# Kernel optimization log

Measured on AMD Instinct MI355X. Metric: run time of the kernel, lower is better.

The kernel has to match this reference:

```python
import jax, jax.numpy as jnp
import numpy as np

B, S, D = 2, 2048, 1024
H, HD = 16, 64  # num_heads, head_dim; H*HD == D


def setup_inputs() -> dict:
    key = jax.random.key(0)
    ks = jax.random.split(key, 10)
    scale = 1.0 / np.sqrt(D)
    inputs_q = jax.random.normal(ks[0], (B, S, D), dtype=jnp.float32)
    inputs_kv = inputs_q  # self-attention
    Wq = jax.random.normal(ks[1], (D, H, HD), dtype=jnp.float32) * scale
    Wk = jax.random.normal(ks[2], (D, H, HD), dtype=jnp.float32) * scale
    Wv = jax.random.normal(ks[3], (D, H, HD), dtype=jnp.float32) * scale
    Wo = jax.random.normal(ks[4], (H, HD, D), dtype=jnp.float32) * scale
    bq = jnp.zeros((H, HD), dtype=jnp.float32)
    bk = jnp.zeros((H, HD), dtype=jnp.float32)
    bv = jnp.zeros((H, HD), dtype=jnp.float32)
    bo = jnp.zeros((D,), dtype=jnp.float32)
    return {"inputs_q": inputs_q, "inputs_kv": inputs_kv,
            "Wq": Wq, "bq": bq, "Wk": Wk, "bk": bk,
            "Wv": Wv, "bv": bv, "Wo": Wo, "bo": bo}


def reference(inputs_q, inputs_kv, Wq, bq, Wk, bk, Wv, bv, Wo, bo):
    # QKV projections: [B,S,D] x [D,H,HD] -> [B,S,H,HD]
    q = jnp.einsum('bsd,dhe->bshe', inputs_q, Wq) + bq
    k = jnp.einsum('bsd,dhe->bshe', inputs_kv, Wk) + bk
    v = jnp.einsum('bsd,dhe->bshe', inputs_kv, Wv) + bv
    # scale query by sqrt(depth) as in dot_product_attention
    q = q / jnp.sqrt(jnp.asarray(HD, dtype=q.dtype))
    # attention scores: [B,H,Sq,Sk]
    scores = jnp.einsum('bqhd,bkhd->bhqk', q, k)
    weights = jax.nn.softmax(scores, axis=-1)
    # weighted values: [B,Sq,H,HD]
    ctx = jnp.einsum('bhqk,bkhd->bqhd', weights, v)
    # output projection over (head, head_dim) axes
    out = jnp.einsum('bqhd,hde->bqe', ctx, Wo) + bo
    return out
```

## Files before the change

kernel.cpp:

```cpp
#include <hip/hip_runtime.h>
#include <hip/hip_bf16.h>

typedef __bf16 bf16x8 __attribute__((ext_vector_type(8)));
typedef __bf16 bf16x4 __attribute__((ext_vector_type(4)));
typedef float f32x4 __attribute__((ext_vector_type(4)));

#define MFMA(a,b,c) __builtin_amdgcn_mfma_f32_16x16x32_bf16(a,b,c,0,0,0)

__device__ __forceinline__ unsigned short f2bf(float f) {
    union { float f; unsigned u; } x; x.f = f;
    unsigned r = x.u + 0x7fffu + ((x.u >> 16) & 1u);
    return (unsigned short)(r >> 16);
}

__device__ __forceinline__ bf16x8 ld8(const unsigned short* p) {
    return *reinterpret_cast<const bf16x8*>(p);
}

__device__ __forceinline__ float exp2_fast(float x) {
    float r; asm("v_exp_f32 %0, %1" : "=v"(r) : "v"(x)); return r;
}

__device__ __forceinline__ void stage16(const unsigned short* g, unsigned short* l) {
    __builtin_amdgcn_global_load_lds(
        (const __attribute__((address_space(1))) unsigned int*)(const void*)(g),
        (__attribute__((address_space(3))) unsigned int*)(void*)(l),
        16, 0, 0);
}

__global__ void k_cvt(const float* __restrict__ in, unsigned short* __restrict__ out, int n4) {
    int i = blockIdx.x * blockDim.x + threadIdx.x;
    int stride = gridDim.x * blockDim.x;
    for (; i < n4; i += stride) {
        float4 v = reinterpret_cast<const float4*>(in)[i];
        ushort4 o;
        o.x = f2bf(v.x); o.y = f2bf(v.y); o.z = f2bf(v.z); o.w = f2bf(v.w);
        reinterpret_cast<ushort4*>(out)[i] = o;
    }
}

__global__ void k_cvt_t(const float* __restrict__ in, unsigned short* __restrict__ out) {
    __shared__ unsigned short tile[64][66];
    int t = threadIdx.x;
    int bk = (blockIdx.x & 15) * 64, bn = (blockIdx.x >> 4) * 64;
    #pragma unroll
    for (int r = 0; r < 16; ++r) {
        int k = (t >> 6) * 16 + r;
        int n = t & 63;
        tile[n][k] = f2bf(in[(bk + k) * 1024 + bn + n]);
    }
    __syncthreads();
    #pragma unroll
    for (int r = 0; r < 16; ++r) {
        int n = (t >> 6) * 16 + r;
        int k = t & 63;
        out[(bn + n) * 1024 + bk + k] = tile[n][k];
    }
}

template<int EPI>
__global__ __launch_bounds__(256) void k_gemm_s(
    const unsigned short* __restrict__ A,
    const unsigned short* __restrict__ Bt,
    const float* __restrict__ b0, const float* __restrict__ b1,
    const float* __restrict__ b2,
    unsigned short* __restrict__ q_out, unsigned short* __restrict__ k_out,
    unsigned short* __restrict__ v_out, float* __restrict__ f_out,
    int M, int N, int K)
{
    __shared__ __align__(16) unsigned short A_lds[2][128][32];
    __shared__ __align__(16) unsigned short B_lds[2][128][32];

    const int lane = threadIdx.x & 63;
    const int wave = threadIdx.x >> 6;
    const int wr = wave >> 1, wc = wave & 1;
    const int nbm = M >> 7;
    const int nwg = nbm * (N >> 7);
    int blk = blockIdx.x;
    blk = (blk & 7) * (nwg >> 3) + (blk >> 3);
    const int bm = (blk % nbm) << 7;
    const int bn = (blk / nbm) << 7;
    const int g = lane >> 4, r16 = lane & 15;

    const int srow = lane >> 2;
    const int schunk = lane & 3;
    const unsigned short* Asrc = A  + (size_t)(bm + wave * 32 + srow) * K + schunk * 8;
    const unsigned short* Bsrc = Bt + (size_t)(bn + wave * 32 + srow) * K + schunk * 8;

    auto stage = [&](int buf, int k0) {
        #pragma unroll
        for (int j = 0; j < 2; ++j) {
            stage16(Asrc + (size_t)(j * 16) * K + k0, &A_lds[buf][wave * 32 + j * 16][0]);
            stage16(Bsrc + (size_t)(j * 16) * K + k0, &B_lds[buf][wave * 32 + j * 16][0]);
        }
    };

    f32x4 acc[4][4] = {};

    stage(0, 0);
    __syncthreads();

    const int nsteps = K >> 5;
    for (int t = 0; t < nsteps; ++t) {
        const int cur = t & 1;
        if (t + 1 < nsteps) stage(cur ^ 1, (t + 1) * 32);

        bf16x8 a[4], b[4];
        #pragma unroll
        for (int i = 0; i < 4; ++i)
            a[i] = ld8(&A_lds[cur][wr * 64 + i * 16 + r16][g * 8]);
        #pragma unroll
        for (int j = 0; j < 4; ++j)
            b[j] = ld8(&B_lds[cur][wc * 64 + j * 16 + r16][g * 8]);
        #pragma unroll
        for (int i = 0; i < 4; ++i)
            #pragma unroll
            for (int j = 0; j < 4; ++j)
                acc[i][j] = MFMA(a[i], b[j], acc[i][j]);
        __syncthreads();
    }

    const int seg = bn >> 10;
    const float* bias = (EPI == 1) ? b0 : (seg == 0 ? b0 : (seg == 1 ? b1 : b2));
    const float scale = (EPI == 0 && seg == 0) ? 0.18033688011112042f : 1.0f;

    #pragma unroll
    for (int i = 0; i < 4; ++i)
        #pragma unroll
        for (int j = 0; j < 4; ++j) {
            const int mbase = bm + wr * 64 + i * 16 + g * 4;
            const int n = bn + wc * 64 + j * 16 + r16;
            if constexpr (EPI == 1) {
                #pragma unroll
                for (int r = 0; r < 4; ++r)
                    f_out[(size_t)(mbase + r) * N + n] = acc[i][j][r] + b0[n];
            } else {
                const int nl = n & 1023;
                const int h = nl >> 6, e = nl & 63;
                const int b_ = mbase >> 11, s0 = mbase & 2047;
                float vv[4];
                #pragma unroll
                for (int r = 0; r < 4; ++r)
                    vv[r] = (acc[i][j][r] + bias[nl]) * scale;
                if (seg == 2) {
                    bf16x4 pk = { (__bf16)vv[0], (__bf16)vv[1], (__bf16)vv[2], (__bf16)vv[3] };
                    *reinterpret_cast<bf16x4*>(
                        &v_out[(((size_t)(b_ * 16 + h) * 64 + e) * 2048) + s0]) = pk;
                } else {
                    unsigned short* o = (seg == 0) ? q_out : k_out;
                    #pragma unroll
                    for (int r = 0; r < 4; ++r)
                        o[(((size_t)(b_ * 16 + h) * 2048 + (s0 + r)) * 64) + e] = f2bf(vv[r]);
                }
            }
        }
}

__global__ __launch_bounds__(256) void k_attn(
    const unsigned short* __restrict__ Q,
    const unsigned short* __restrict__ Kb,
    const unsigned short* __restrict__ Vt,
    unsigned short* __restrict__ ctx)
{
    __shared__ __align__(16) unsigned short K_lds[2][64][64];
    __shared__ __align__(16) unsigned short V_lds[2][64][64];
    __shared__ __align__(16) unsigned short P_lds[4][32][72];

    const int lane = threadIdx.x & 63;
    const int wave = threadIdx.x >> 6;
    const int g = lane >> 4, r16 = lane & 15;

    const int blk = blockIdx.x;
    const int x = blk & 7, i = blk >> 3;
    const int bh = x * 4 + (i & 3);
    const int qb = i >> 2;
    const int b = bh >> 4, h = bh & 15;
    const int q0 = qb * 128 + wave * 32;

    const unsigned short* Qp    = Q  + ((size_t)bh * 2048 + q0) * 64;
    const unsigned short* Khead = Kb + (size_t)bh * 2048 * 64;
    const unsigned short* Vhead = Vt + (size_t)bh * 64 * 2048;

    bf16x8 aq[2][2];
    #pragma unroll
    for (int m = 0; m < 2; ++m)
        #pragma unroll
        for (int h2 = 0; h2 < 2; ++h2)
            aq[m][h2] = ld8(Qp + (size_t)(m * 16 + r16) * 64 + h2 * 32 + g * 8);

    bf16x8 ones;
    #pragma unroll
    for (int j = 0; j < 8; ++j) ones[j] = (__bf16)1.0f;

    const int srow = lane >> 3;
    const int schunk = (lane & 7) ^ srow;

    auto stage = [&](int buf, int kt) {
        #pragma unroll
        for (int j = 0; j < 2; ++j) {
            const int r0 = wave * 16 + j * 8;
            stage16(Khead + (size_t)(kt + r0 + srow) * 64 + schunk * 8,
                    &K_lds[buf][r0][0]);
            stage16(Vhead + (size_t)(r0 + srow) * 2048 + kt + schunk * 8,
                    &V_lds[buf][r0][0]);
        }
    };

    f32x4 o[2][4] = {};
    f32x4 sum_acc[2] = {};
    const int sw = r16 & 7;

    stage(0, 0);
    __syncthreads();

    for (int it = 0; it < 32; ++it) {
        const int cur = it & 1;
        if (it + 1 < 32) stage(cur ^ 1, (it + 1) * 64);

        f32x4 s[2][4] = {};
        #pragma unroll
        for (int c = 0; c < 4; ++c) {
            bf16x8 bk0 = ld8(&K_lds[cur][c * 16 + r16][((g)     ^ sw) * 8]);
            bf16x8 bk1 = ld8(&K_lds[cur][c * 16 + r16][((4 + g) ^ sw) * 8]);
            #pragma unroll
            for (int m = 0; m < 2; ++m) {
                s[m][c] = MFMA(bk0, aq[m][0], s[m][c]);
                s[m][c] = MFMA(bk1, aq[m][1], s[m][c]);
            }
        }
        bf16x8 bv[4][2];
        #pragma unroll
        for (int n = 0; n < 4; ++n)
            #pragma unroll
            for (int ks = 0; ks < 2; ++ks)
                bv[n][ks] = ld8(&V_lds[cur][n * 16 + r16][((ks * 4 + g) ^ sw) * 8]);

        #pragma unroll
        for (int m = 0; m < 2; ++m) {
            #pragma unroll
            for (int c = 0; c < 4; ++c) {
                float p0 = exp2_fast(s[m][c][0]);
                float p1 = exp2_fast(s[m][c][1]);
                float p2 = exp2_fast(s[m][c][2]);
                float p3 = exp2_fast(s[m][c][3]);
                bf16x4 pk = { (__bf16)p0, (__bf16)p1, (__bf16)p2, (__bf16)p3 };
                *reinterpret_cast<bf16x4*>(&P_lds[wave][m * 16 + r16][c * 16 + g * 4]) = pk;
            }
        }
        #pragma unroll
        for (int m = 0; m < 2; ++m) {
            bf16x8 ap0 = ld8(&P_lds[wave][m * 16 + r16][g * 8]);
            bf16x8 ap1 = ld8(&P_lds[wave][m * 16 + r16][32 + g * 8]);
            #pragma unroll
            for (int n = 0; n < 4; ++n) {
                o[m][n] = MFMA(ap0, bv[n][0], o[m][n]);
                o[m][n] = MFMA(ap1, bv[n][1], o[m][n]);
            }
            sum_acc[m] = MFMA(ap0, ones, sum_acc[m]);
            sum_acc[m] = MFMA(ap1, ones, sum_acc[m]);
        }
        __syncthreads();
    }

    #pragma unroll
    for (int m = 0; m < 2; ++m) {
        float inv[4];
        #pragma unroll
        for (int r = 0; r < 4; ++r) inv[r] = 1.0f / sum_acc[m][r];
        #pragma unroll
        for (int n = 0; n < 4; ++n)
            #pragma unroll
            for (int r = 0; r < 4; ++r) {
                int q = q0 + m * 16 + g * 4 + r;
                float v = o[m][n][r] * inv[r];
                ctx[((size_t)(b * 2048 + q)) * 1024 + h * 64 + n * 16 + r16] = f2bf(v);
            }
    }
}

extern "C" void kernel_launch(void* const* d_in, const int* in_sizes, int n_in,
                              void* d_out, int out_size, void* d_ws, size_t ws_size,
                              hipStream_t stream)
{
    const float* xq  = (const float*)d_in[0];
    const float* Wq  = (const float*)d_in[2];
    const float* bq  = (const float*)d_in[3];
    const float* Wk  = (const float*)d_in[4];
    const float* bk  = (const float*)d_in[5];
    const float* Wv  = (const float*)d_in[6];
    const float* bv  = (const float*)d_in[7];
    const float* Wo  = (const float*)d_in[8];
    const float* bo  = (const float*)d_in[9];
    float* out = (float*)d_out;

    char* ws = (char*)d_ws;
    const size_t MB = 1024 * 1024;
    unsigned short* Xq_b   = (unsigned short*)(ws + 0);
    unsigned short* Wqkvt  = (unsigned short*)(ws + 16 * MB);
    unsigned short* Wot    = (unsigned short*)(ws + 22 * MB);
    unsigned short* Qb     = (unsigned short*)(ws + 24 * MB);
    unsigned short* Kbuf   = (unsigned short*)(ws + 32 * MB);
    unsigned short* Vt     = (unsigned short*)(ws + 40 * MB);
    unsigned short* Ctx    = (unsigned short*)(ws + 48 * MB);

    k_cvt<<<1024, 256, 0, stream>>>(xq, Xq_b, (4096 * 1024) / 4);
    k_cvt_t<<<256, 256, 0, stream>>>(Wq, Wqkvt);
    k_cvt_t<<<256, 256, 0, stream>>>(Wk, Wqkvt + 1024 * 1024);
    k_cvt_t<<<256, 256, 0, stream>>>(Wv, Wqkvt + 2 * 1024 * 1024);
    k_cvt_t<<<256, 256, 0, stream>>>(Wo, Wot);

    k_gemm_s<0><<<768, 256, 0, stream>>>(Xq_b, Wqkvt, bq, bk, bv,
                                         Qb, Kbuf, Vt, nullptr, 4096, 3072, 1024);

    k_attn<<<512, 256, 0, stream>>>(Qb, Kbuf, Vt, Ctx);

    k_gemm_s<1><<<256, 256, 0, stream>>>(Ctx, Wot, bo, bo, bo,
                                         nullptr, nullptr, nullptr, out, 4096, 1024, 1024);
}
```

Measured before the change: 126.5 us.

## Keep softmax probabilities in registers by permuting K rows and V swizzle

Removes the per-wave P shared-memory round trip by choosing a K row permutation so the QK^T MFMA output layout matches the A-operand layout of the PV MFMA, letting exp2 results be packed directly into bf16x8 registers. The staging XOR swizzle and the K/V read swizzles are changed to stay consistent with the permuted rows. This cuts LDS writes and reads, plus the LDS footprint per block, which may raise occupancy. The cost is more complex indexing, and correctness depends on the permutation matching the V column order exactly.

```diff
diff --git a/kernel.cpp b/kernel.cpp
--- a/kernel.cpp
+++ b/kernel.cpp
@@ -164,7 +164,6 @@
 {
     __shared__ __align__(16) unsigned short K_lds[2][64][64];
     __shared__ __align__(16) unsigned short V_lds[2][64][64];
-    __shared__ __align__(16) unsigned short P_lds[4][32][72];
 
     const int lane = threadIdx.x & 63;
     const int wave = threadIdx.x >> 6;
@@ -193,22 +192,25 @@
     for (int j = 0; j < 8; ++j) ones[j] = (__bf16)1.0f;
 
     const int srow = lane >> 3;
-    const int schunk = (lane & 7) ^ srow;
 
     auto stage = [&](int buf, int kt) {
         #pragma unroll
         for (int j = 0; j < 2; ++j) {
             const int r0 = wave * 16 + j * 8;
-            stage16(Khead + (size_t)(kt + r0 + srow) * 64 + schunk * 8,
+            const int sc = (lane & 7) ^ (srow & 3) ^ (j << 2);
+            stage16(Khead + (size_t)(kt + r0 + srow) * 64 + sc * 8,
                     &K_lds[buf][r0][0]);
-            stage16(Vhead + (size_t)(r0 + srow) * 2048 + kt + schunk * 8,
+            stage16(Vhead + (size_t)(r0 + srow) * 2048 + kt + sc * 8,
                     &V_lds[buf][r0][0]);
         }
     };
 
     f32x4 o[2][4] = {};
     f32x4 sum_acc[2] = {};
-    const int sw = r16 & 7;
+
+    const int krow_base = (r16 >> 2) * 8 + (r16 & 3);
+    const int pik = (r16 & 3) | (((r16 >> 2) & 1) << 2);
+    const int piv = (r16 & 3) | (((r16 >> 3) & 1) << 2);
 
     stage(0, 0);
     __syncthreads();
@@ -220,8 +222,9 @@
         f32x4 s[2][4] = {};
         #pragma unroll
         for (int c = 0; c < 4; ++c) {
-            bf16x8 bk0 = ld8(&K_lds[cur][c * 16 + r16][((g)     ^ sw) * 8]);
-            bf16x8 bk1 = ld8(&K_lds[cur][c * 16 + r16][((4 + g) ^ sw) * 8]);
+            const int krow = 32 * (c >> 1) + (c & 1) * 4 + krow_base;
+            bf16x8 bk0 = ld8(&K_lds[cur][krow][((g)     ^ pik) * 8]);
+            bf16x8 bk1 = ld8(&K_lds[cur][krow][((4 + g) ^ pik) * 8]);
             #pragma unroll
             for (int m = 0; m < 2; ++m) {
                 s[m][c] = MFMA(bk0, aq[m][0], s[m][c]);
@@ -233,24 +236,18 @@
         for (int n = 0; n < 4; ++n)
             #pragma unroll
             for (int ks = 0; ks < 2; ++ks)
-                bv[n][ks] = ld8(&V_lds[cur][n * 16 + r16][((ks * 4 + g) ^ sw) * 8]);
+                bv[n][ks] = ld8(&V_lds[cur][n * 16 + r16][((ks * 4 + g) ^ piv) * 8]);
 
         #pragma unroll
         for (int m = 0; m < 2; ++m) {
-            #pragma unroll
-            for (int c = 0; c < 4; ++c) {
-                float p0 = exp2_fast(s[m][c][0]);
-                float p1 = exp2_fast(s[m][c][1]);
-                float p2 = exp2_fast(s[m][c][2]);
-                float p3 = exp2_fast(s[m][c][3]);
-                bf16x4 pk = { (__bf16)p0, (__bf16)p1, (__bf16)p2, (__bf16)p3 };
-                *reinterpret_cast<bf16x4*>(&P_lds[wave][m * 16 + r16][c * 16 + g * 4]) = pk;
-            }
-        }
-        #pragma unroll
-        for (int m = 0; m < 2; ++m) {
-            bf16x8 ap0 = ld8(&P_lds[wave][m * 16 + r16][g * 8]);
-            bf16x8 ap1 = ld8(&P_lds[wave][m * 16 + r16][32 + g * 8]);
+            bf16x8 ap0, ap1;
+            #pragma unroll
+            for (int r = 0; r < 4; ++r) {
+                ap0[r]     = (__bf16)exp2_fast(s[m][0][r]);
+                ap0[4 + r] = (__bf16)exp2_fast(s[m][1][r]);
+                ap1[r]     = (__bf16)exp2_fast(s[m][2][r]);
+                ap1[4 + r] = (__bf16)exp2_fast(s[m][3][r]);
+            }
             #pragma unroll
             for (int n = 0; n < 4; ++n) {
                 o[m][n] = MFMA(ap0, bv[n][0], o[m][n]);
```

Result: faster. 121.9 us (-3.6%).
